# Performance work log

Measured on AMD Instinct MI355X. Metric: run time of the kernel, lower is better.

The kernel has to match this reference:

```python
import jax, jax.numpy as jnp
import numpy as np


def _gru(x, w_ih, w_hh, b_ih, b_hh, reverse=False):
    # PyTorch GRU cell math. x: (N, T, Din) -> (N, T, Hh)
    N, T, _ = x.shape
    Hh = w_hh.shape[1]
    xp = jnp.einsum('ntd,gd->ntg', x, w_ih) + b_ih  # (N, T, 3*Hh), input gates precomputed

    def step(h, xp_t):
        gh = h @ w_hh.T + b_hh
        ir, iz, inn = jnp.split(xp_t, 3, axis=-1)
        hr, hz, hn = jnp.split(gh, 3, axis=-1)
        r = jax.nn.sigmoid(ir + hr)
        z = jax.nn.sigmoid(iz + hz)
        n = jnp.tanh(inn + r * hn)
        h_new = (1.0 - z) * n + z * h
        return h_new, h_new

    h0 = jnp.zeros((N, Hh), x.dtype)
    _, ys = jax.lax.scan(step, h0, jnp.swapaxes(xp, 0, 1), reverse=reverse)
    return jnp.swapaxes(ys, 0, 1)


def _bigru(x, pf, pb):
    return jnp.concatenate([_gru(x, *pf), _gru(x, *pb, reverse=True)], axis=-1)


def _attn(out, w, b, ctx):
    # out: (N, T, H). tanh(Linear) -> context dot -> softmax -> weighted sum
    u = jnp.tanh(jnp.einsum('nth,gh->ntg', out, w) + b)
    a = jax.nn.softmax(u @ ctx, axis=-1)  # (N, T)
    return jnp.einsum('nt,nth->nh', a, out)


def setup_inputs() -> dict:
    key = jax.random.key(0)
    H, Hh = 512, 256
    S, B, Nsent = 2048, 16, 16
    L = S // Nsent
    ks = jax.random.split(key, 32)

    def p(k, shape):
        return jax.random.normal(k, shape, jnp.float32) * 0.05

    starts = jnp.arange(Nsent, dtype=jnp.int32) * L
    spans = jnp.stack([starts, starts + L], axis=-1)  # (Nsent, 2)
    spans = jnp.broadcast_to(spans, (B, Nsent, 2))

    inp = {
        'token_feats': jax.random.normal(ks[0], (S, B, H), jnp.float32),
        'sentence_spans': spans,
        # word BiGRU params (forward / backward directions)
        'w_wih_f': p(ks[1], (3 * Hh, H)), 'w_whh_f': p(ks[2], (3 * Hh, Hh)),
        'w_bih_f': p(ks[3], (3 * Hh,)), 'w_bhh_f': p(ks[4], (3 * Hh,)),
        'w_wih_b': p(ks[5], (3 * Hh, H)), 'w_whh_b': p(ks[6], (3 * Hh, Hh)),
        'w_bih_b': p(ks[7], (3 * Hh,)), 'w_bhh_b': p(ks[8], (3 * Hh,)),
        # sentence BiGRU params
        's_wih_f': p(ks[9], (3 * Hh, H)), 's_whh_f': p(ks[10], (3 * Hh, Hh)),
        's_bih_f': p(ks[11], (3 * Hh,)), 's_bhh_f': p(ks[12], (3 * Hh,)),
        's_wih_b': p(ks[13], (3 * Hh, H)), 's_whh_b': p(ks[14], (3 * Hh, Hh)),
        's_bih_b': p(ks[15], (3 * Hh,)), 's_bhh_b': p(ks[16], (3 * Hh,)),
        # attention params
        'w_attn_w': p(ks[17], (H, H)), 'w_attn_b': p(ks[18], (H,)),
        'w_ctx': jax.random.normal(ks[19], (H,), jnp.float32),
        's_attn_w': p(ks[20], (H, H)), 's_attn_b': p(ks[21], (H,)),
        's_ctx': jax.random.normal(ks[22], (H,), jnp.float32),
    }
    return inp


def reference(token_feats, sentence_spans,
              w_wih_f, w_whh_f, w_bih_f, w_bhh_f,
              w_wih_b, w_whh_b, w_bih_b, w_bhh_b,
              s_wih_f, s_whh_f, s_bih_f, s_bhh_f,
              s_wih_b, s_whh_b, s_bih_b, s_bhh_b,
              w_attn_w, w_attn_b, w_ctx,
              s_attn_w, s_attn_b, s_ctx):
    S, B, H = token_feats.shape
    Nsent = sentence_spans.shape[1]
    L = S // Nsent  # uniform spans: segment b,i = tokens [i*L, (i+1)*L)

    x = jnp.swapaxes(token_feats, 0, 1)  # (B, S, H)
    segs = x.reshape(B * Nsent, L, H)    # all sentences batched together

    # word-level BiGRU + word attention -> sentence vectors
    out_w = _bigru(segs, (w_wih_f, w_whh_f, w_bih_f, w_bhh_f),
                   (w_wih_b, w_whh_b, w_bih_b, w_bhh_b))  # (B*Nsent, L, H)
    sent_vecs = _attn(out_w, w_attn_w, w_attn_b, w_ctx).reshape(B, Nsent, H)

    # sentence-level BiGRU + sentence attention (no padding: all masks true)
    out_s = _bigru(sent_vecs, (s_wih_f, s_whh_f, s_bih_f, s_bhh_f),
                   (s_wih_b, s_whh_b, s_bih_b, s_bhh_b))  # (B, Nsent, H)
    Yh = _attn(out_s, s_attn_w, s_attn_b, s_ctx)  # (B, H)
    return Yh
```

## Files before the change

kernel.cpp:

```cpp
#include <hip/hip_runtime.h>
#include <stdint.h>


using uint32  = unsigned int;
using bf16x8  = __attribute__((ext_vector_type(8))) __bf16;
using floatx4 = __attribute__((ext_vector_type(4))) float;

__device__ __forceinline__ float b2f(unsigned short u) {
    union { uint32 i; float f; } v; v.i = ((uint32)u) << 16; return v.f;
}
__device__ __forceinline__ unsigned short f2b(float f) {
    union { float f; uint32 i; } v; v.f = f;
    uint32 r = v.i + 0x7fffu + ((v.i >> 16) & 1u);
    return (unsigned short)(r >> 16);
}
__device__ __forceinline__ float sigmoidf_(float x) { return 1.f / (1.f + __expf(-x)); }
__device__ __forceinline__ float tanhf_(float x) {
    x = fminf(15.f, fmaxf(-15.f, x));
    float e = __expf(2.f * x);
    return (e - 1.f) / (e + 1.f);
}

__device__ __forceinline__ void gl16(const unsigned short* g, unsigned short* l) {
    __builtin_amdgcn_global_load_lds(
        (const __attribute__((address_space(1))) uint32*)g,
        (__attribute__((address_space(3))) uint32*)l, 16, 0, 0);
}

#define O_XPC     0L
#define O_OWHI    50331648L
#define O_OWLO    83886080L
#define O_STATE   117440512L
#define O_SCW     117964800L
#define O_W0HI    118095872L
#define O_W0LO    118882304L
#define O_W1HI    119668736L
#define O_W1LO    120455168L
#define O_WAHI    121241600L
#define O_WALO    121765888L
#define O_S0HI    122290176L
#define O_S0LO    123076608L
#define O_S1HI    123863040L
#define O_S1LO    124649472L
#define O_SAHI    125435904L
#define O_SALO    125960192L
#define O_HW0     126484480L
#define O_HW1     126877696L
#define O_HS0     127270912L
#define O_HS1     127664128L
#define O_SENTHI  128057344L
#define O_SENTLO  128319488L
#define O_XPS     128581632L
#define O_SSTATE  130154496L
#define O_OSHI    130187264L
#define O_OSLO    130449408L
#define O_SCS     130711552L
#define O_TKWH    130712576L
#define O_TKWL    164267008L

__global__ __launch_bounds__(256)
void cvt_hilo6(const float* __restrict__ s0, const float* __restrict__ s1,
               const float* __restrict__ s2, const float* __restrict__ s3,
               const float* __restrict__ s4, const float* __restrict__ s5,
               char* __restrict__ ws)
{
    const int b = blockIdx.x;
    const float* src; unsigned short *hi, *lo; int base;
    if (b < 192)      { src = s0; hi = (unsigned short*)(ws + O_W0HI); lo = (unsigned short*)(ws + O_W0LO); base = b; }
    else if (b < 384) { src = s1; hi = (unsigned short*)(ws + O_W1HI); lo = (unsigned short*)(ws + O_W1LO); base = b - 192; }
    else if (b < 576) { src = s2; hi = (unsigned short*)(ws + O_S0HI); lo = (unsigned short*)(ws + O_S0LO); base = b - 384; }
    else if (b < 768) { src = s3; hi = (unsigned short*)(ws + O_S1HI); lo = (unsigned short*)(ws + O_S1LO); base = b - 576; }
    else if (b < 896) { src = s4; hi = (unsigned short*)(ws + O_WAHI); lo = (unsigned short*)(ws + O_WALO); base = b - 768; }
    else              { src = s5; hi = (unsigned short*)(ws + O_SAHI); lo = (unsigned short*)(ws + O_SALO); base = b - 896; }
    const int idx = (base * 256 + threadIdx.x) * 8;
    float f[8];
    *reinterpret_cast<float4*>(&f[0]) = *reinterpret_cast<const float4*>(src + idx);
    *reinterpret_cast<float4*>(&f[4]) = *reinterpret_cast<const float4*>(src + idx + 4);
    unsigned short h[8], l[8];
    #pragma unroll
    for (int j = 0; j < 8; ++j) {
        h[j] = f2b(f[j]);
        l[j] = f2b(f[j] - b2f(h[j]));
    }
    *reinterpret_cast<uint4*>(hi + idx) = *reinterpret_cast<const uint4*>(h);
    *reinterpret_cast<uint4*>(lo + idx) = *reinterpret_cast<const uint4*>(l);
}

__global__ __launch_bounds__(256)
void cvt_b4(const float* __restrict__ s0, const float* __restrict__ s1,
            const float* __restrict__ s2, const float* __restrict__ s3,
            char* __restrict__ ws)
{
    const int b = blockIdx.x;
    const float* src; unsigned short* dst; int base;
    if (b < 96)       { src = s0; dst = (unsigned short*)(ws + O_HW0); base = b; }
    else if (b < 192) { src = s1; dst = (unsigned short*)(ws + O_HW1); base = b - 96; }
    else if (b < 288) { src = s2; dst = (unsigned short*)(ws + O_HS0); base = b - 192; }
    else              { src = s3; dst = (unsigned short*)(ws + O_HS1); base = b - 288; }
    const int idx = (base * 256 + threadIdx.x) * 8;
    float f[8];
    *reinterpret_cast<float4*>(&f[0]) = *reinterpret_cast<const float4*>(src + idx);
    *reinterpret_cast<float4*>(&f[4]) = *reinterpret_cast<const float4*>(src + idx + 4);
    unsigned short o[8];
    #pragma unroll
    for (int j = 0; j < 8; ++j) o[j] = f2b(f[j]);
    *reinterpret_cast<uint4*>(dst + idx) = *reinterpret_cast<const uint4*>(o);
}

__global__ __launch_bounds__(256)
void cvt_tokfull(const float* __restrict__ tok, unsigned short* __restrict__ whi,
                 unsigned short* __restrict__ wlo)
{
    const int u = blockIdx.x * 256 + threadIdx.x;
    const int h8 = u & 63;
    const int rest = u >> 6;
    const int t = rest & 127, seq = rest >> 7;
    const int sent = seq & 15, b = seq >> 4;
    const long src = ((long)(sent * 128 + t) * 16 + b) * 512 + h8 * 8;
    float f[8];
    *reinterpret_cast<float4*>(&f[0]) = *reinterpret_cast<const float4*>(tok + src);
    *reinterpret_cast<float4*>(&f[4]) = *reinterpret_cast<const float4*>(tok + src + 4);
    unsigned short h[8], l[8];
    #pragma unroll
    for (int j = 0; j < 8; ++j) {
        h[j] = f2b(f[j]);
        l[j] = f2b(f[j] - b2f(h[j]));
    }
    const long dst = (long)rest * 512 + h8 * 8;
    *reinterpret_cast<uint4*>(whi + dst) = *reinterpret_cast<const uint4*>(h);
    *reinterpret_cast<uint4*>(wlo + dst) = *reinterpret_cast<const uint4*>(l);
}

template<int AMODE>
__device__ __forceinline__ long amap(int m, int t0, int sgn) {
    if (AMODE == 1) {
        const int sq = m >> 5, tl = m & 31;
        return (long)(sq * 128 + t0 + sgn * tl) * 512;
    } else if (AMODE == 3) {
        const int n = m >> 4, tl = m & 15;
        return (long)(n * 16 + t0 + sgn * tl) * 512;
    }
    return (long)m * 512;
}

template<int AMODE, int OUT>
__global__ __launch_bounds__(256)
void gemm_d(const unsigned short* __restrict__ Ahi, const unsigned short* __restrict__ Alo,
            const unsigned short* __restrict__ Wh0, const unsigned short* __restrict__ Wl0,
            const unsigned short* __restrict__ Wh1, const unsigned short* __restrict__ Wl1,
            const float* __restrict__ b0, const float* __restrict__ b1,
            float* __restrict__ C, int ldC, long c1off,
            float* __restrict__ score, const float* __restrict__ ctx,
            int t00, int t01, int nbyHalf)
{
    __shared__ __align__(16) unsigned short smem[2 * 16384];

    int bx = blockIdx.x, by = blockIdx.y;
    {
        const int nbx = gridDim.x, nby = gridDim.y;
        if ((nby & 7) == 0) {
            const int l = by * nbx + bx;
            const int xcd = l & 7;
            const int s = l >> 3;
            bx = s % nbx;
            by = xcd * (nby >> 3) + s / nbx;
        }
    }

    const int tid  = threadIdx.x;
    const int lane = tid & 63;
    const int wave = tid >> 6;
    const int wm = wave >> 1, wn = wave & 1;
    const int n_base = bx * 128;
    const int q = lane >> 4;
    const int r = lane & 15;

    const unsigned short* Whi = Wh0;
    const unsigned short* Wlo = Wl0;
    const float* bias = b0;
    float* Cb = C;
    int t0 = t00, sgn = 1, m_base;
    if (nbyHalf > 0 && by >= nbyHalf) {
        Whi = Wh1; Wlo = Wl1; bias = b1; Cb = C + c1off;
        t0 = t01; sgn = -1;
        m_base = (by - nbyHalf) * 128;
    } else {
        m_base = by * 128;
    }

    long aoff[2], woff[2];
    #pragma unroll
    for (int i = 0; i < 2; ++i) {
        const int s = tid + 256 * i;
        const int R = s >> 2, kg = s & 3;
        const int kq = (kg - (R >> 1)) & 3;
        aoff[i] = amap<AMODE>(m_base + R, t0, sgn) + kq * 8;
        woff[i] = (long)(n_base + R) * 512 + kq * 8;
    }

    floatx4 acc[4][4];
    #pragma unroll
    for (int mt = 0; mt < 4; ++mt)
        #pragma unroll
        for (int nt = 0; nt < 4; ++nt) acc[mt][nt] = (floatx4){0.f, 0.f, 0.f, 0.f};

    auto stage = [&](int ts) {
        const int k0 = ts * 32;
        unsigned short* B = smem + (ts & 1) * 16384;
        #pragma unroll
        for (int i = 0; i < 2; ++i) {
            const int ld = (tid + 256 * i) * 8;
            gl16(Ahi + aoff[i] + k0, B + ld);
            gl16(Alo + aoff[i] + k0, B + 4096 + ld);
            gl16(Whi + woff[i] + k0, B + 8192 + ld);
            gl16(Wlo + woff[i] + k0, B + 12288 + ld);
        }
    };

    stage(0);
    for (int t = 0; t < 16; ++t) {
        stage(t + 1 < 16 ? t + 1 : 15);
        asm volatile("s_waitcnt vmcnt(8)\n\ts_barrier" ::: "memory");

        const unsigned short* B = smem + (t & 1) * 16384;
        bf16x8 ah[4], al[4];
        #pragma unroll
        for (int mt = 0; mt < 4; ++mt) {
            const int R = wm * 64 + mt * 16 + r;
            const int s = R * 4 + ((q + (R >> 1)) & 3);
            ah[mt] = *reinterpret_cast<const bf16x8*>(B + s * 8);
            al[mt] = *reinterpret_cast<const bf16x8*>(B + 4096 + s * 8);
        }
        #pragma unroll
        for (int nt = 0; nt < 4; ++nt) {
            const int Rn = wn * 64 + nt * 16 + r;
            const int sn = Rn * 4 + ((q + (Rn >> 1)) & 3);
            bf16x8 wh = *reinterpret_cast<const bf16x8*>(B + 8192 + sn * 8);
            bf16x8 wl = *reinterpret_cast<const bf16x8*>(B + 12288 + sn * 8);
            #pragma unroll
            for (int mt = 0; mt < 4; ++mt) {
                acc[mt][nt] = __builtin_amdgcn_mfma_f32_16x16x32_bf16(ah[mt], wh, acc[mt][nt], 0, 0, 0);
                acc[mt][nt] = __builtin_amdgcn_mfma_f32_16x16x32_bf16(ah[mt], wl, acc[mt][nt], 0, 0, 0);
                acc[mt][nt] = __builtin_amdgcn_mfma_f32_16x16x32_bf16(al[mt], wh, acc[mt][nt], 0, 0, 0);
            }
        }
        asm volatile("s_waitcnt lgkmcnt(0)\n\ts_barrier" ::: "memory");
    }
    asm volatile("s_waitcnt vmcnt(0)" ::: "memory");

    if (OUT == 0) {
        #pragma unroll
        for (int nt = 0; nt < 4; ++nt) {
            const int n = n_base + wn * 64 + nt * 16 + r;
            const float bs = bias[n];
            #pragma unroll
            for (int mt = 0; mt < 4; ++mt) {
                const int m = m_base + wm * 64 + mt * 16 + q * 4;
                #pragma unroll
                for (int e = 0; e < 4; ++e)
                    Cb[(long)(m + e) * ldC + n] = acc[mt][nt][e] + bs;
            }
        }
    } else {
        #pragma unroll
        for (int mt = 0; mt < 4; ++mt) {
            float p[4] = {0.f, 0.f, 0.f, 0.f};
            #pragma unroll
            for (int nt = 0; nt < 4; ++nt) {
                const int n = n_base + wn * 64 + nt * 16 + r;
                const float cx = ctx[n];
                const float bs = bias[n];
                #pragma unroll
                for (int e = 0; e < 4; ++e)
                    p[e] += cx * tanhf_(acc[mt][nt][e] + bs);
            }
            #pragma unroll
            for (int mk = 1; mk < 16; mk <<= 1) {
                #pragma unroll
                for (int e = 0; e < 4; ++e) p[e] += __shfl_xor(p[e], mk, 64);
            }
            if (r == 0) {
                const int m = m_base + wm * 64 + mt * 16 + q * 4;
                #pragma unroll
                for (int e = 0; e < 4; ++e)
                    atomicAdd(&score[m + e], p[e]);
            }
        }
    }
}

__global__ __launch_bounds__(512, 2)
void gru2(const float* __restrict__ xp,
          const unsigned short* __restrict__ Wf,
          const unsigned short* __restrict__ Wb,
          const float* __restrict__ bhf, const float* __restrict__ bhb,
          float* __restrict__ state,
          unsigned short* __restrict__ ohi, unsigned short* __restrict__ olo,
          int steps, int t0f, int t0b, int groups, int Tout)
{
    __shared__ float pre[768 * 5];
    __shared__ unsigned short Bf[8 * 64 * 8];

    const int tid  = threadIdx.x;
    const int lane = tid & 63;
    const int w    = tid >> 6;
    const int dir  = blockIdx.x / groups;
    const int g    = blockIdx.x % groups;
    const int nseq = groups * 2;
    const unsigned short* W = dir ? Wb : Wf;
    const float* bh = dir ? bhb : bhf;
    const int t0  = dir ? t0b : t0f;
    const int sgn = dir ? -1 : 1;

    const int s = tid >> 8;
    const int j = tid & 255;
    const float bhr = bh[j], bhz = bh[j + 256], bhn = bh[j + 512];

    bf16x8 wf[6][8];
    {
        const int r0 = w * 96 + (lane & 15);
        const int kf = (lane >> 4) * 8;
        #pragma unroll
        for (int mt = 0; mt < 6; ++mt)
            #pragma unroll
            for (int kk = 0; kk < 8; ++kk)
                wf[mt][kk] = *reinterpret_cast<const bf16x8*>(
                    W + (long)(r0 + mt * 16) * 256 + kk * 32 + kf);
    }

    #pragma unroll
    for (int i = 0; i < 4; ++i)
        reinterpret_cast<uint32*>(Bf)[tid * 4 + i] = 0;

    float h = state[((long)dir * nseq + g * 2 + s) * 256 + j];
    const int posHi = ((j >> 5) * 64 + ((j >> 3) & 3) * 16 + s) * 8 + (j & 7);
    const int posLo = ((j >> 5) * 64 + ((j >> 3) & 3) * 16 + 2 + s) * 8 + (j & 7);
    {
        const unsigned short hb = f2b(h);
        Bf[posHi] = hb;
        Bf[posLo] = f2b(h - b2f(hb));
    }
    asm volatile("s_waitcnt lgkmcnt(0)\n\ts_barrier" ::: "memory");

    const float* xbase = xp + (long)dir * nseq * steps * 768
                       + (long)(g * 2 + s) * steps * 768;
    const int q = lane >> 4, r = lane & 15;

    float xr = xbase[j], xz = xbase[256 + j], xn = xbase[512 + j];

    for (int st = 0; st < steps; ++st) {
        const int t = t0 + sgn * st;

        const int sn = (st + 1 < steps) ? st + 1 : st;
        const float* xb = xbase + (long)sn * 768;
        const float nxr = xb[j];
        const float nxz = xb[256 + j];
        const float nxn = xb[512 + j];

        floatx4 acc[6];
        #pragma unroll
        for (int mt = 0; mt < 6; ++mt) acc[mt] = (floatx4){0.f, 0.f, 0.f, 0.f};
        #pragma unroll
        for (int kk = 0; kk < 8; ++kk) {
            bf16x8 bv = *reinterpret_cast<const bf16x8*>(Bf + (kk * 64 + lane) * 8);
            #pragma unroll
            for (int mt = 0; mt < 6; ++mt)
                acc[mt] = __builtin_amdgcn_mfma_f32_16x16x32_bf16(wf[mt][kk], bv, acc[mt], 0, 0, 0);
        }
        if (r < 4) {
            #pragma unroll
            for (int mt = 0; mt < 6; ++mt) {
                const int row = w * 96 + mt * 16 + q * 4;
                #pragma unroll
                for (int e = 0; e < 4; ++e)
                    pre[(row + e) * 5 + r] = acc[mt][e];
            }
        }
        asm volatile("s_waitcnt lgkmcnt(0)\n\ts_barrier" ::: "memory");

        {
            const float pr = pre[j * 5 + s]         + pre[j * 5 + 2 + s];
            const float pz = pre[(j + 256) * 5 + s] + pre[(j + 256) * 5 + 2 + s];
            const float pn = pre[(j + 512) * 5 + s] + pre[(j + 512) * 5 + 2 + s];
            const float rg = sigmoidf_(xr + pr + bhr);
            const float zg = sigmoidf_(xz + pz + bhz);
            const float nn = tanhf_(xn + rg * (pn + bhn));
            h = (1.f - zg) * nn + zg * h;
            const unsigned short hb = f2b(h);
            const unsigned short lb = f2b(h - b2f(hb));
            Bf[posHi] = hb;
            Bf[posLo] = lb;
            const long orow = ((long)(g * 2 + s) * Tout + t) * 512 + dir * 256 + j;
            ohi[orow] = hb;
            olo[orow] = lb;
        }
        xr = nxr; xz = nxz; xn = nxn;
        asm volatile("s_waitcnt lgkmcnt(0)\n\ts_barrier" ::: "memory");
    }

    state[((long)dir * nseq + g * 2 + s) * 256 + j] = h;
}

template<int MODE, int T>
__global__ __launch_bounds__(256)
void attn_wsum(const float* __restrict__ score,
               const unsigned short* __restrict__ fhi,
               const unsigned short* __restrict__ flo,
               void* __restrict__ o1, void* __restrict__ o2)
{
    const int n = blockIdx.x;
    const int tid = threadIdx.x;
    __shared__ float a[T];
    __shared__ float e[T];
    if (tid < T) a[tid] = score[n * T + tid];
    __syncthreads();
    float mx = -1e30f;
    #pragma unroll
    for (int t = 0; t < T; ++t) mx = fmaxf(mx, a[t]);
    if (tid < T) e[tid] = __expf(a[tid] - mx);
    __syncthreads();
    float sm = 0.f;
    #pragma unroll
    for (int t = 0; t < T; ++t) sm += e[t];
    const float inv = 1.f / sm;
    float acc0 = 0.f, acc1 = 0.f;
    #pragma unroll 8
    for (int t = 0; t < T; ++t) {
        const float w = e[t] * inv;
        const long base = ((long)n * T + t) * 512;
        acc0 += w * (b2f(fhi[base + tid])       + b2f(flo[base + tid]));
        acc1 += w * (b2f(fhi[base + tid + 256]) + b2f(flo[base + tid + 256]));
    }
    if (MODE == 1) {
        float* o = (float*)o1;
        o[n * 512 + tid] = acc0;
        o[n * 512 + tid + 256] = acc1;
    } else {
        unsigned short* oh = (unsigned short*)o1;
        unsigned short* ol = (unsigned short*)o2;
        const unsigned short h0 = f2b(acc0), h1 = f2b(acc1);
        oh[n * 512 + tid]       = h0;  ol[n * 512 + tid]       = f2b(acc0 - b2f(h0));
        oh[n * 512 + tid + 256] = h1;  ol[n * 512 + tid + 256] = f2b(acc1 - b2f(h1));
    }
}

extern "C" void kernel_launch(void* const* d_in, const int* in_sizes, int n_in,
                              void* d_out, int out_size, void* d_ws, size_t ws_size,
                              hipStream_t stream) {
    const float* tok      = (const float*)d_in[0];
    const float* w_wih_f  = (const float*)d_in[2];
    const float* w_whh_f  = (const float*)d_in[3];
    const float* w_bih_f  = (const float*)d_in[4];
    const float* w_bhh_f  = (const float*)d_in[5];
    const float* w_wih_b  = (const float*)d_in[6];
    const float* w_whh_b  = (const float*)d_in[7];
    const float* w_bih_b  = (const float*)d_in[8];
    const float* w_bhh_b  = (const float*)d_in[9];
    const float* s_wih_f  = (const float*)d_in[10];
    const float* s_whh_f  = (const float*)d_in[11];
    const float* s_bih_f  = (const float*)d_in[12];
    const float* s_bhh_f  = (const float*)d_in[13];
    const float* s_wih_b  = (const float*)d_in[14];
    const float* s_whh_b  = (const float*)d_in[15];
    const float* s_bih_b  = (const float*)d_in[16];
    const float* s_bhh_b  = (const float*)d_in[17];
    const float* w_attn_b = (const float*)d_in[19];
    const float* w_ctx    = (const float*)d_in[20];
    const float* s_attn_b = (const float*)d_in[22];
    const float* s_ctx    = (const float*)d_in[23];

    char* ws = (char*)d_ws;
    float*          xpc   = (float*)(ws + O_XPC);
    unsigned short* owhi  = (unsigned short*)(ws + O_OWHI);
    unsigned short* owlo  = (unsigned short*)(ws + O_OWLO);
    float*          state = (float*)(ws + O_STATE);
    float*          score_w = (float*)(ws + O_SCW);
    unsigned short* W0HI  = (unsigned short*)(ws + O_W0HI);
    unsigned short* W0LO  = (unsigned short*)(ws + O_W0LO);
    unsigned short* W1HI  = (unsigned short*)(ws + O_W1HI);
    unsigned short* W1LO  = (unsigned short*)(ws + O_W1LO);
    unsigned short* WAHI  = (unsigned short*)(ws + O_WAHI);
    unsigned short* WALO  = (unsigned short*)(ws + O_WALO);
    unsigned short* S0HI  = (unsigned short*)(ws + O_S0HI);
    unsigned short* S0LO  = (unsigned short*)(ws + O_S0LO);
    unsigned short* S1HI  = (unsigned short*)(ws + O_S1HI);
    unsigned short* S1LO  = (unsigned short*)(ws + O_S1LO);
    unsigned short* SAHI  = (unsigned short*)(ws + O_SAHI);
    unsigned short* SALO  = (unsigned short*)(ws + O_SALO);
    unsigned short* HW0   = (unsigned short*)(ws + O_HW0);
    unsigned short* HW1   = (unsigned short*)(ws + O_HW1);
    unsigned short* HS0   = (unsigned short*)(ws + O_HS0);
    unsigned short* HS1   = (unsigned short*)(ws + O_HS1);
    unsigned short* senthi = (unsigned short*)(ws + O_SENTHI);
    unsigned short* sentlo = (unsigned short*)(ws + O_SENTLO);
    float*          xp_s  = (float*)(ws + O_XPS);
    float*          sstate = (float*)(ws + O_SSTATE);
    unsigned short* oshi  = (unsigned short*)(ws + O_OSHI);
    unsigned short* oslo  = (unsigned short*)(ws + O_OSLO);
    float*          score_s = (float*)(ws + O_SCS);
    unsigned short* tkwh  = (unsigned short*)(ws + O_TKWH);
    unsigned short* tkwl  = (unsigned short*)(ws + O_TKWL);

    const dim3 blk(256);

    hipMemsetAsync(ws + O_STATE,  0, 524288, stream);
    hipMemsetAsync(ws + O_SSTATE, 0, 32768, stream);
    hipMemsetAsync(ws + O_SCW,    0, 131072, stream);
    hipMemsetAsync(ws + O_SCS,    0, 1024, stream);

    cvt_hilo6<<<dim3(1024), blk, 0, stream>>>(w_wih_f, w_wih_b, s_wih_f, s_wih_b,
                                              (const float*)d_in[18], (const float*)d_in[21], ws);
    cvt_b4<<<dim3(384), blk, 0, stream>>>(w_whh_f, w_whh_b, s_whh_f, s_whh_b, ws);
    cvt_tokfull<<<dim3(8192), blk, 0, stream>>>(tok, tkwh, tkwl);

    const long XDW = 256L * 32 * 768;
    for (int c = 0; c < 4; ++c) {
        gemm_d<1, 0><<<dim3(6, 128), blk, 0, stream>>>(
            tkwh, tkwl, W0HI, W0LO, W1HI, W1LO, w_bih_f, w_bih_b,
            xpc, 768, XDW, nullptr, nullptr, 32 * c, 127 - 32 * c, 64);
        gru2<<<dim3(256), dim3(512), 0, stream>>>(
            xpc, HW0, HW1, w_bhh_f, w_bhh_b, state, owhi, owlo,
            32, 32 * c, 127 - 32 * c, 128, 128);
    }

    gemm_d<2, 1><<<dim3(4, 256), blk, 0, stream>>>(
        owhi, owlo, WAHI, WALO, WAHI, WALO, w_attn_b, w_attn_b,
        nullptr, 0, 0, score_w, w_ctx, 0, 0, 0);
    attn_wsum<0, 128><<<dim3(256), blk, 0, stream>>>(score_w, owhi, owlo, senthi, sentlo);

    const long XDS = 16L * 16 * 768;
    gemm_d<3, 0><<<dim3(6, 4), blk, 0, stream>>>(
        senthi, sentlo, S0HI, S0LO, S1HI, S1LO, s_bih_f, s_bih_b,
        xp_s, 768, XDS, nullptr, nullptr, 0, 15, 2);

    gru2<<<dim3(16), dim3(512), 0, stream>>>(
        xp_s, HS0, HS1, s_bhh_f, s_bhh_b, sstate, oshi, oslo,
        16, 0, 15, 8, 16);

    gemm_d<2, 1><<<dim3(4, 2), blk, 0, stream>>>(
        oshi, oslo, SAHI, SALO, SAHI, SALO, s_attn_b, s_attn_b,
        nullptr, 0, 0, score_s, s_ctx, 0, 0, 0);
    attn_wsum<1, 16><<<dim3(16), blk, 0, stream>>>(score_s, oshi, oslo, d_out, nullptr);
}
```

Measured before the change: 687.7 us.

## Add 256x256-tile split-bf16 GEMM with 512 threads for word-level projections

Adds a new GEMM kernel that computes a 256x256 output tile per 512-thread block, with each wave owning a 128x64 sub-tile, in place of the previous 256-thread kernel. It is used for the word-level input-gate projection and the word-attention score GEMM. The larger tile raises operand reuse and cuts global and LDS traffic per MFMA. In exchange it uses twice the LDS (128 KB double-buffered) and a 128-float accumulator per thread, which can limit occupancy, and the grid shrinks to 192 or 256 blocks, which may underfill the GPU.

Result: no change. 694.6 us (+1.0%).

```diff
diff --git a/kernel.cpp b/kernel.cpp
--- a/kernel.cpp
+++ b/kernel.cpp
@@ -141,6 +141,156 @@
         return (long)(n * 16 + t0 + sgn * tl) * 512;
     }
     return (long)m * 512;
+}
+
+template<int AMODE, int OUT>
+__global__ __launch_bounds__(512, 2)
+void gemm_t(const unsigned short* __restrict__ Ahi, const unsigned short* __restrict__ Alo,
+            const unsigned short* __restrict__ Wh0, const unsigned short* __restrict__ Wl0,
+            const unsigned short* __restrict__ Wh1, const unsigned short* __restrict__ Wl1,
+            const float* __restrict__ b0, const float* __restrict__ b1,
+            float* __restrict__ C, int ldC, long c1off,
+            float* __restrict__ score, const float* __restrict__ ctx,
+            int t00, int t01, int nbyHalf)
+{
+    __shared__ __align__(16) unsigned short smem[2 * 32768];
+
+    int bx = blockIdx.x, by = blockIdx.y;
+    {
+        const int nbx = gridDim.x, nby = gridDim.y;
+        if ((nby & 7) == 0) {
+            const int l = by * nbx + bx;
+            const int xcd = l & 7;
+            const int s = l >> 3;
+            bx = s % nbx;
+            by = xcd * (nby >> 3) + s / nbx;
+        }
+    }
+
+    const int tid  = threadIdx.x;
+    const int lane = tid & 63;
+    const int wave = tid >> 6;
+    const int wm = wave >> 2, wn = wave & 3;
+    const int n_base = bx * 256;
+    const int q = lane >> 4;
+    const int r = lane & 15;
+
+    const unsigned short* Whi = Wh0;
+    const unsigned short* Wlo = Wl0;
+    const float* bias = b0;
+    float* Cb = C;
+    int t0 = t00, sgn = 1, m_base;
+    if (nbyHalf > 0 && by >= nbyHalf) {
+        Whi = Wh1; Wlo = Wl1; bias = b1; Cb = C + c1off;
+        t0 = t01; sgn = -1;
+        m_base = (by - nbyHalf) * 256;
+    } else {
+        m_base = by * 256;
+    }
+
+    long aoff[2], woff[2];
+    #pragma unroll
+    for (int i = 0; i < 2; ++i) {
+        const int s = tid + 512 * i;
+        const int R = s >> 2, kg = s & 3;
+        const int kq = (kg - (R >> 1)) & 3;
+        aoff[i] = amap<AMODE>(m_base + R, t0, sgn) + kq * 8;
+        woff[i] = (long)(n_base + R) * 512 + kq * 8;
+    }
+
+    floatx4 acc[8][4];
+    #pragma unroll
+    for (int mt = 0; mt < 8; ++mt)
+        #pragma unroll
+        for (int nt = 0; nt < 4; ++nt) acc[mt][nt] = (floatx4){0.f, 0.f, 0.f, 0.f};
+
+    auto stage = [&](int ts) {
+        const int k0 = ts * 32;
+        unsigned short* B = smem + (ts & 1) * 32768;
+        #pragma unroll
+        for (int i = 0; i < 2; ++i) {
+            const int ld = (tid + 512 * i) * 8;
+            gl16(Ahi + aoff[i] + k0, B + ld);
+            gl16(Alo + aoff[i] + k0, B + 8192 + ld);
+            gl16(Whi + woff[i] + k0, B + 16384 + ld);
+            gl16(Wlo + woff[i] + k0, B + 24576 + ld);
+        }
+    };
+
+    stage(0);
+    for (int t = 0; t < 16; ++t) {
+        stage(t + 1 < 16 ? t + 1 : 15);
+        asm volatile("s_waitcnt vmcnt(8)\n\ts_barrier" ::: "memory");
+
+        const unsigned short* B  = smem + (t & 1) * 32768;
+        const unsigned short* BAl = B + 8192;
+        const unsigned short* BW  = B + 16384;
+        const unsigned short* BWl = B + 24576;
+
+        bf16x8 wh[4], wl[4];
+        #pragma unroll
+        for (int nt = 0; nt < 4; ++nt) {
+            const int Rn = wn * 64 + nt * 16 + r;
+            const int sn = Rn * 4 + ((q + (Rn >> 1)) & 3);
+            wh[nt] = *reinterpret_cast<const bf16x8*>(BW  + sn * 8);
+            wl[nt] = *reinterpret_cast<const bf16x8*>(BWl + sn * 8);
+        }
+        #pragma unroll
+        for (int mt = 0; mt < 8; ++mt) {
+            const int R = wm * 128 + mt * 16 + r;
+            const int s = R * 4 + ((q + (R >> 1)) & 3);
+            const bf16x8 ah = *reinterpret_cast<const bf16x8*>(B   + s * 8);
+            const bf16x8 al = *reinterpret_cast<const bf16x8*>(BAl + s * 8);
+            #pragma unroll
+            for (int nt = 0; nt < 4; ++nt) {
+                acc[mt][nt] = __builtin_amdgcn_mfma_f32_16x16x32_bf16(ah, wh[nt], acc[mt][nt], 0, 0, 0);
+                acc[mt][nt] = __builtin_amdgcn_mfma_f32_16x16x32_bf16(ah, wl[nt], acc[mt][nt], 0, 0, 0);
+                acc[mt][nt] = __builtin_amdgcn_mfma_f32_16x16x32_bf16(al, wh[nt], acc[mt][nt], 0, 0, 0);
+            }
+        }
+        asm volatile("s_waitcnt lgkmcnt(0)\n\ts_barrier" ::: "memory");
+    }
+    asm volatile("s_waitcnt vmcnt(0)" ::: "memory");
+
+    if (OUT == 0) {
+        #pragma unroll
+        for (int nt = 0; nt < 4; ++nt) {
+            const int n = n_base + wn * 64 + nt * 16 + r;
+            const float bs = bias[n];
+            #pragma unroll
+            for (int mt = 0; mt < 8; ++mt) {
+                const int m = m_base + wm * 128 + mt * 16 + q * 4;
+                #pragma unroll
+                for (int e = 0; e < 4; ++e)
+                    Cb[(long)(m + e) * ldC + n] = acc[mt][nt][e] + bs;
+            }
+        }
+    } else {
+        #pragma unroll
+        for (int mt = 0; mt < 8; ++mt) {
+            float p[4] = {0.f, 0.f, 0.f, 0.f};
+            #pragma unroll
+            for (int nt = 0; nt < 4; ++nt) {
+                const int n = n_base + wn * 64 + nt * 16 + r;
+                const float cx = ctx[n];
+                const float bs = bias[n];
+                #pragma unroll
+                for (int e = 0; e < 4; ++e)
+                    p[e] += cx * tanhf_(acc[mt][nt][e] + bs);
+            }
+            #pragma unroll
+            for (int mk = 1; mk < 16; mk <<= 1) {
+                #pragma unroll
+                for (int e = 0; e < 4; ++e) p[e] += __shfl_xor(p[e], mk, 64);
+            }
+            if (r == 0) {
+                const int m = m_base + wm * 128 + mt * 16 + q * 4;
+                #pragma unroll
+                for (int e = 0; e < 4; ++e)
+                    atomicAdd(&score[m + e], p[e]);
+            }
+        }
+    }
 }
 
 template<int AMODE, int OUT>
@@ -515,15 +665,15 @@
 
     const long XDW = 256L * 32 * 768;
     for (int c = 0; c < 4; ++c) {
-        gemm_d<1, 0><<<dim3(6, 128), blk, 0, stream>>>(
+        gemm_t<1, 0><<<dim3(3, 64), dim3(512), 0, stream>>>(
             tkwh, tkwl, W0HI, W0LO, W1HI, W1LO, w_bih_f, w_bih_b,
-            xpc, 768, XDW, nullptr, nullptr, 32 * c, 127 - 32 * c, 64);
+            xpc, 768, XDW, nullptr, nullptr, 32 * c, 127 - 32 * c, 32);
         gru2<<<dim3(256), dim3(512), 0, stream>>>(
             xpc, HW0, HW1, w_bhh_f, w_bhh_b, state, owhi, owlo,
             32, 32 * c, 127 - 32 * c, 128, 128);
     }
 
-    gemm_d<2, 1><<<dim3(4, 256), blk, 0, stream>>>(
+    gemm_t<2, 1><<<dim3(2, 128), dim3(512), 0, stream>>>(
         owhi, owlo, WAHI, WALO, WAHI, WALO, w_attn_b, w_attn_b,
         nullptr, 0, 0, score_w, w_ctx, 0, 0, 0);
     attn_wsum<0, 128><<<dim3(256), blk, 0, stream>>>(score_w, owhi, owlo, senthi, sentlo);
```
